# Kernel tuning notes

Measured on AMD Instinct MI355X. Metric: run time of the kernel, lower is better.

Reference implementation:

```python
import jax, jax.numpy as jnp
import numpy as np

N, E = 50000, 400000
IC, OC, WIDTH, DEPTH = 128, 128, 2, 3


def setup_inputs() -> dict:
    key = jax.random.key(0)
    ks = jax.random.split(key, 9)
    s = 0.02
    return {
        "node_tensor": jax.random.normal(ks[0], (N, 1, IC), jnp.float32),
        "edge_index": jax.random.randint(ks[1], (2, E), 0, N, dtype=jnp.int32),
        "W_pre": jax.random.normal(ks[2], (IC, OC * WIDTH), jnp.float32) * s,
        "b_pre": jax.random.normal(ks[3], (OC * WIDTH,), jnp.float32) * s,
        "W_merge": jax.random.normal(ks[4], (IC, OC * WIDTH), jnp.float32) * s,
        "b_merge": jax.random.normal(ks[5], (OC * WIDTH,), jnp.float32) * s,
        "W_conv": jax.random.normal(ks[6], (WIDTH, OC, OC), jnp.float32) * s,
        "b_conv": jax.random.normal(ks[7], (OC * WIDTH,), jnp.float32) * s,
    }


def reference(node_tensor, edge_index, W_pre, b_pre, W_merge, b_merge, W_conv, b_conv):
    n = node_tensor.shape[0]
    nodes = node_tensor[:, 0, :]                       # (N, IC)

    src, dst = edge_index[0], edge_index[1]
    deg = jax.ops.segment_sum(jnp.ones((E,), node_tensor.dtype), dst, num_segments=n)
    norm = jnp.where(deg > 0, jax.lax.rsqrt(jnp.maximum(deg, 1.0)), 0.0)  # D^{-1/2}

    def laplacian_action(x):                           # x: (N, C); L_sym x
        agg = jax.ops.segment_sum(norm[src, None] * x[src], dst, num_segments=n)
        return x - norm[:, None] * agg

    merge = nodes @ W_merge + b_merge                  # (N, OC*W)
    out = jax.nn.relu(nodes @ W_pre + b_pre + merge)   # (N, OC*W)

    for _ in range(DEPTH - 1):
        out = out - laplacian_action(out)
        # grouped 1x1 conv: width contiguous groups of OC channels
        h = out.reshape(n, WIDTH, OC)
        h = jnp.einsum("nwi,woi->nwo", h, W_conv).reshape(n, WIDTH * OC) + b_conv
        out = jax.nn.relu(h + merge)

    # final (N, OC, W) reshape + adaptive_avg_pool1d(1) == mean over width
    out = out.reshape(n, OC, WIDTH).mean(axis=-1)
    return out[:, :, None]                             # (N, OC, 1)
```

## Files before the change

### kernel.cpp

```cpp
#include <hip/hip_runtime.h>

typedef unsigned short u16;
typedef __attribute__((ext_vector_type(8))) short bf16x8;
typedef __attribute__((ext_vector_type(4))) float f32x4;

#define ICNST 128
#define C2 256

__device__ __forceinline__ float bf2f(u16 u){
  return __uint_as_float(((unsigned int)u) << 16);
}
__device__ __forceinline__ float2 bf2x2(unsigned int u){
  float2 r;
  r.x = __uint_as_float(u << 16);
  r.y = __uint_as_float(u & 0xffff0000u);
  return r;
}
__device__ __forceinline__ u16 f2bf(float f){
  unsigned int u = __float_as_uint(f);
  unsigned int r = (u + 0x7fffu + ((u >> 16) & 1u)) >> 16;
  return (u16)r;
}
__device__ __forceinline__ unsigned int pk2(float a, float b){
  return (unsigned int)f2bf(a) | ((unsigned int)f2bf(b) << 16);
}

__global__ __launch_bounds__(512) void k_zero(int* __restrict__ deg, int n){
  int i = blockIdx.x * 512 + threadIdx.x;
  if (i < n) deg[i] = 0;
}

__global__ __launch_bounds__(256) void k_pre(const int* __restrict__ dst,
    int* __restrict__ deg, const float* __restrict__ Wpre,
    const float* __restrict__ Wmrg, const float* __restrict__ Wcv,
    u16* __restrict__ WT, u16* __restrict__ Wc, int E){
  int bid = blockIdx.x;
  if (bid < 384){
    int idx = bid * 256 + threadIdx.x;
    if (idx < 65536){
      int j = idx & 511, k = idx >> 9;
      float v = (j < 256) ? Wpre[k * 256 + j] : Wmrg[k * 256 + (j - 256)];
      WT[j * 128 + k] = f2bf(v);
    } else if (idx < 65536 + 32768){
      int x = idx - 65536;
      Wc[x] = f2bf(Wcv[x]);
    }
  } else {
    int e = (bid - 384) * 256 + threadIdx.x;
    if (e < E) atomicAdd(&deg[dst[e]], 1);
  }
}

__global__ __launch_bounds__(256) void k_scan1(const int* __restrict__ deg,
    int* __restrict__ bsum, int n){
  __shared__ int red[256];
  int t = threadIdx.x;
  int i = blockIdx.x * 256 + t;
  red[t] = (i < n) ? deg[i] : 0;
  __syncthreads();
  for (int off = 128; off > 0; off >>= 1){
    if (t < off) red[t] += red[t + off];
    __syncthreads();
  }
  if (t == 0) bsum[blockIdx.x] = red[0];
}

__global__ __launch_bounds__(256) void k_scan2(int* __restrict__ bsum, int nb){
  __shared__ int s[256];
  int t = threadIdx.x;
  int v = (t < nb) ? bsum[t] : 0;
  s[t] = v;
  __syncthreads();
  for (int off = 1; off < 256; off <<= 1){
    int u = (t >= off) ? s[t - off] : 0;
    __syncthreads();
    s[t] += u;
    __syncthreads();
  }
  if (t < nb) bsum[t] = s[t] - v;
}

__global__ __launch_bounds__(256) void k_scan3(const int* __restrict__ deg,
    const int* __restrict__ bsum, int* __restrict__ row_start,
    int* __restrict__ cursor, float* __restrict__ norm, int n){
  __shared__ int s[256];
  int t = threadIdx.x;
  int i = blockIdx.x * 256 + t;
  int v = (i < n) ? deg[i] : 0;
  s[t] = v;
  __syncthreads();
  for (int off = 1; off < 256; off <<= 1){
    int u = (t >= off) ? s[t - off] : 0;
    __syncthreads();
    s[t] += u;
    __syncthreads();
  }
  int ex = s[t] - v + bsum[blockIdx.x];
  if (i < n){
    row_start[i] = ex;
    cursor[i] = ex;
    norm[i] = (v > 0) ? rsqrtf((float)v) : 0.f;
    if (i == n - 1) row_start[n] = ex + v;
  }
}

__global__ void k_scatter(const int* __restrict__ src, const int* __restrict__ dstA,
    int* __restrict__ cursor, int* __restrict__ csr_src, int E){
  int e = blockIdx.x * blockDim.x + threadIdx.x;
  if (e < E){
    int d = dstA[e];
    int pos = atomicAdd(&cursor[d], 1);
    csr_src[pos] = src[e];
  }
}

__global__ __launch_bounds__(512) void k_initM(const float* __restrict__ node,
    const u16* __restrict__ WT, const float* __restrict__ bpre,
    const float* __restrict__ bmrg, const float* __restrict__ norm,
    u16* __restrict__ merge, u16* __restrict__ outA, int n){
  __shared__ u16 Al[64 * 128];
  __shared__ u16 Ep[64 * 256];
  int t = threadIdx.x;
  int w = t >> 6, l = t & 63;
  int n0 = blockIdx.x * 64;
  int cb = w * 32;
  int lk = (l >> 4) * 8;

  float nr4[4];
  #pragma unroll
  for (int fr = 0; fr < 4; ++fr){
    int row = n0 + fr * 16 + (l & 15);
    nr4[fr] = (row < n) ? norm[row] : 0.f;
  }
  float4 bPr[2], bMr[2];
  #pragma unroll
  for (int fcp = 0; fcp < 2; ++fcp){
    int j0 = cb + fcp * 16 + (l >> 4) * 4;
    bPr[fcp] = *(const float4*)(bpre + j0);
    bMr[fcp] = *(const float4*)(bmrg + j0);
  }

  {
    int row = t >> 3, c0 = (t & 7) * 16;
    const float* src = node + (size_t)(n0 + row) * ICNST + c0;
    bool ok = (n0 + row) < n;
    #pragma unroll
    for (int q = 0; q < 4; ++q){
      float4 v = ok ? *(const float4*)(src + q * 4) : float4{0.f, 0.f, 0.f, 0.f};
      int byte = (row * 256 + c0 * 2 + q * 8) ^ ((row & 7) << 4);
      uint2 pp; pp.x = pk2(v.x, v.y); pp.y = pk2(v.z, v.w);
      *(uint2*)((char*)Al + byte) = pp;
    }
  }
  __syncthreads();

  f32x4 acc[4][4] = {};
  #pragma unroll
  for (int ks = 0; ks < 4; ++ks){
    bf16x8 bf[4];
    #pragma unroll
    for (int fc = 0; fc < 4; ++fc){
      int j = (fc < 2) ? (cb + fc * 16 + (l & 15))
                       : (256 + cb + (fc - 2) * 16 + (l & 15));
      bf[fc] = *(const bf16x8*)(WT + (size_t)j * 128 + ks * 32 + lk);
    }
    bf16x8 af[4];
    #pragma unroll
    for (int fr = 0; fr < 4; ++fr){
      int row = fr * 16 + (l & 15);
      int byte = (row * 256 + ks * 64 + (l >> 4) * 16) ^ ((l & 7) << 4);
      af[fr] = *(const bf16x8*)((const char*)Al + byte);
    }
    #pragma unroll
    for (int fr = 0; fr < 4; ++fr)
      #pragma unroll
      for (int fc = 0; fc < 4; ++fc)
        acc[fr][fc] = __builtin_amdgcn_mfma_f32_16x16x32_bf16(bf[fc], af[fr], acc[fr][fc], 0, 0, 0);
  }

  #pragma unroll
  for (int fr = 0; fr < 4; ++fr){
    int rl = fr * 16 + (l & 15);
    int row = n0 + rl;
    bool ok = row < n;
    float nr = nr4[fr];
    #pragma unroll
    for (int fcp = 0; fcp < 2; ++fcp){
      int j0 = cb + fcp * 16 + (l >> 4) * 4;
      f32x4 aP = acc[fr][fcp], aM = acc[fr][fcp + 2];
      float bPe[4] = {bPr[fcp].x, bPr[fcp].y, bPr[fcp].z, bPr[fcp].w};
      float bMe[4] = {bMr[fcp].x, bMr[fcp].y, bMr[fcp].z, bMr[fcp].w};
      ushort4 mgv, outv;
      u16* mgp = (u16*)&mgv; u16* otp = (u16*)&outv;
      #pragma unroll
      for (int r = 0; r < 4; ++r){
        float mg = aM[r] + bMe[r];
        float o  = aP[r] + bPe[r] + mg;
        o = (o > 0.f) ? o : 0.f;
        mgp[r] = f2bf(mg);
        otp[r] = f2bf(nr * o);
      }
      if (ok) *(ushort4*)(merge + (size_t)row * C2 + j0) = mgv;
      int byte = (rl * 512 + j0 * 2) ^ ((rl & 7) << 4);
      *(ushort4*)((char*)Ep + byte) = outv;
    }
  }
  __syncthreads();
  #pragma unroll
  for (int round = 0; round < 4; ++round){
    int idx = round * 512 + t;
    int rl = idx >> 5, off = (idx & 31) * 16;
    int byte = (rl * 512 + off) ^ ((rl & 7) << 4);
    uint4 v = *(const uint4*)((const char*)Ep + byte);
    if (n0 + rl < n)
      *(uint4*)((char*)outA + (size_t)(n0 + rl) * 512 + off) = v;
  }
}

template<int FINAL>
__global__ __launch_bounds__(512) void k_convM(u16* __restrict__ buf,
    const u16* __restrict__ Wc, const float* __restrict__ bc,
    const u16* __restrict__ merge, const float* __restrict__ norm,
    float* __restrict__ out, int n){
  __shared__ u16 Al[64 * 256];
  __shared__ u16 Ep[64 * 256];
  int t = threadIdx.x;
  int w = t >> 6, l = t & 63;
  int n0 = blockIdx.x * 64;
  int wh = w >> 2;
  int lk = (l >> 4) * 8;

  float nr4[4];
  #pragma unroll
  for (int fr = 0; fr < 4; ++fr){
    int row = n0 + fr * 16 + (l & 15);
    nr4[fr] = (row < n) ? norm[row] : 0.f;
  }
  float4 bCr[2];
  #pragma unroll
  for (int fc = 0; fc < 2; ++fc)
    bCr[fc] = *(const float4*)(bc + w * 32 + fc * 16 + (l >> 4) * 4);

  {
    int row = t >> 3, c0 = (t & 7) * 32;
    bool ok = (n0 + row) < n;
    const u16* srcA = buf   + (size_t)(n0 + row) * C2 + c0;
    const u16* srcM = merge + (size_t)(n0 + row) * C2 + c0;
    #pragma unroll
    for (int q = 0; q < 4; ++q){
      uint4 va = ok ? *(const uint4*)(srcA + q * 8) : uint4{0u, 0u, 0u, 0u};
      int byte = (row * 512 + c0 * 2 + q * 16) ^ ((row & 7) << 4);
      *(uint4*)((char*)Al + byte) = va;
      uint4 vm = ok ? *(const uint4*)(srcM + q * 8) : uint4{0u, 0u, 0u, 0u};
      *(uint4*)((char*)Ep + byte) = vm;
    }
  }
  __syncthreads();

  f32x4 acc[4][2] = {};
  #pragma unroll
  for (int ks = 0; ks < 4; ++ks){
    bf16x8 bf[2];
    #pragma unroll
    for (int fc = 0; fc < 2; ++fc){
      int rw = w * 32 + fc * 16 + (l & 15);
      bf[fc] = *(const bf16x8*)(Wc + (size_t)rw * 128 + ks * 32 + lk);
    }
    bf16x8 af[4];
    #pragma unroll
    for (int fr = 0; fr < 4; ++fr){
      int row = fr * 16 + (l & 15);
      int byte = (row * 512 + wh * 256 + ks * 64 + (l >> 4) * 16) ^ ((l & 7) << 4);
      af[fr] = *(const bf16x8*)((const char*)Al + byte);
    }
    #pragma unroll
    for (int fr = 0; fr < 4; ++fr)
      #pragma unroll
      for (int fc = 0; fc < 2; ++fc)
        acc[fr][fc] = __builtin_amdgcn_mfma_f32_16x16x32_bf16(bf[fc], af[fr], acc[fr][fc], 0, 0, 0);
  }

  #pragma unroll
  for (int fr = 0; fr < 4; ++fr){
    int rl = fr * 16 + (l & 15);
    float nr = nr4[fr];
    #pragma unroll
    for (int fc = 0; fc < 2; ++fc){
      int j0 = w * 32 + fc * 16 + (l >> 4) * 4;
      int byte = (rl * 512 + j0 * 2) ^ ((rl & 7) << 4);
      ushort4 mg4 = *(const ushort4*)((const char*)Ep + byte);
      const u16* mge = (const u16*)&mg4;
      float bCe[4] = {bCr[fc].x, bCr[fc].y, bCr[fc].z, bCr[fc].w};
      float v[4];
      #pragma unroll
      for (int r = 0; r < 4; ++r){
        float o = acc[fr][fc][r] + bCe[r] + bf2f(mge[r]);
        v[r] = (o > 0.f) ? o : 0.f;
      }
      if (!FINAL){
        ushort4 ov;
        u16* ovp = (u16*)&ov;
        #pragma unroll
        for (int r = 0; r < 4; ++r) ovp[r] = f2bf(nr * v[r]);
        *(ushort4*)((char*)Ep + byte) = ov;
      } else {
        float2 om;
        om.x = 0.5f * (v[0] + v[1]);
        om.y = 0.5f * (v[2] + v[3]);
        *(float2*)((char*)Ep + byte) = om;
      }
    }
  }
  __syncthreads();
  char* dstBase = FINAL ? (char*)out : (char*)buf;
  #pragma unroll
  for (int round = 0; round < 4; ++round){
    int idx = round * 512 + t;
    int rl = idx >> 5, off = (idx & 31) * 16;
    int byte = (rl * 512 + off) ^ ((rl & 7) << 4);
    uint4 v = *(const uint4*)((const char*)Ep + byte);
    if (n0 + rl < n)
      *(uint4*)(dstBase + (size_t)(n0 + rl) * 512 + off) = v;
  }
}

__global__ __launch_bounds__(256) void k_prop(const u16* __restrict__ A, u16* __restrict__ B,
    const int* __restrict__ row_start, const int* __restrict__ csr,
    const float* __restrict__ norm, int n){
  int wid = (blockIdx.x * 256 + threadIdx.x) >> 6;
  int lane = threadIdx.x & 63;
  int half = lane >> 5, c = lane & 31;
  int gw = wid * 2 + half;
  if (gw >= n) return;
  int b = row_start[gw], e = row_start[gw + 1];
  float a0 = 0.f, a1 = 0.f, a2 = 0.f, a3 = 0.f, a4 = 0.f, a5 = 0.f, a6 = 0.f, a7 = 0.f;
  const u16* Ac = A + (size_t)c * 8;
  int j = b;
  for (; j + 4 <= e; j += 4){
    int s0 = csr[j], s1 = csr[j + 1], s2 = csr[j + 2], s3 = csr[j + 3];
    uint4 r0 = *(const uint4*)(Ac + (size_t)s0 * C2);
    uint4 r1 = *(const uint4*)(Ac + (size_t)s1 * C2);
    uint4 r2 = *(const uint4*)(Ac + (size_t)s2 * C2);
    uint4 r3 = *(const uint4*)(Ac + (size_t)s3 * C2);
    float2 p;
    p = bf2x2(r0.x); a0 += p.x; a1 += p.y; p = bf2x2(r0.y); a2 += p.x; a3 += p.y;
    p = bf2x2(r0.z); a4 += p.x; a5 += p.y; p = bf2x2(r0.w); a6 += p.x; a7 += p.y;
    p = bf2x2(r1.x); a0 += p.x; a1 += p.y; p = bf2x2(r1.y); a2 += p.x; a3 += p.y;
    p = bf2x2(r1.z); a4 += p.x; a5 += p.y; p = bf2x2(r1.w); a6 += p.x; a7 += p.y;
    p = bf2x2(r2.x); a0 += p.x; a1 += p.y; p = bf2x2(r2.y); a2 += p.x; a3 += p.y;
    p = bf2x2(r2.z); a4 += p.x; a5 += p.y; p = bf2x2(r2.w); a6 += p.x; a7 += p.y;
    p = bf2x2(r3.x); a0 += p.x; a1 += p.y; p = bf2x2(r3.y); a2 += p.x; a3 += p.y;
    p = bf2x2(r3.z); a4 += p.x; a5 += p.y; p = bf2x2(r3.w); a6 += p.x; a7 += p.y;
  }
  for (; j < e; ++j){
    int s0 = csr[j];
    uint4 r0 = *(const uint4*)(Ac + (size_t)s0 * C2);
    float2 p;
    p = bf2x2(r0.x); a0 += p.x; a1 += p.y; p = bf2x2(r0.y); a2 += p.x; a3 += p.y;
    p = bf2x2(r0.z); a4 += p.x; a5 += p.y; p = bf2x2(r0.w); a6 += p.x; a7 += p.y;
  }
  float nd = norm[gw];
  uint4 ov;
  ov.x = pk2(nd * a0, nd * a1);
  ov.y = pk2(nd * a2, nd * a3);
  ov.z = pk2(nd * a4, nd * a5);
  ov.w = pk2(nd * a6, nd * a7);
  *(uint4*)(B + (size_t)gw * C2 + c * 8) = ov;
}

extern "C" void kernel_launch(void* const* d_in, const int* in_sizes, int n_in,
                              void* d_out, int out_size, void* d_ws, size_t ws_size,
                              hipStream_t stream){
  const float* node = (const float*)d_in[0];
  const int*   eidx = (const int*)d_in[1];
  const float* Wpre = (const float*)d_in[2];
  const float* bpre = (const float*)d_in[3];
  const float* Wmrg = (const float*)d_in[4];
  const float* bmrg = (const float*)d_in[5];
  const float* Wcv  = (const float*)d_in[6];
  const float* bcv  = (const float*)d_in[7];
  float* out = (float*)d_out;

  const int n = in_sizes[0] / ICNST;
  const int E = in_sizes[1] / 2;
  const int* srcp = eidx;
  const int* dstp = eidx + E;

  char* ws = (char*)d_ws;
  size_t off = 0;
  auto alloc = [&](size_t bytes) -> char* {
    char* p = ws + off;
    off += bytes;
    off = (off + 255) & ~(size_t)255;
    return p;
  };
  int*   deg       = (int*)  alloc((size_t)n * 4);
  float* norm      = (float*)alloc((size_t)n * 4);
  int*   row_start = (int*)  alloc((size_t)(n + 1) * 4);
  int*   cursor    = (int*)  alloc((size_t)n * 4);
  int*   csr       = (int*)  alloc((size_t)E * 4);
  u16*   merge     = (u16*)  alloc((size_t)n * C2 * 2);
  u16*   bufA      = (u16*)  alloc((size_t)n * C2 * 2);
  u16*   bufB      = (u16*)  alloc((size_t)n * C2 * 2);
  u16*   WT        = (u16*)  alloc((size_t)512 * 128 * 2);
  u16*   Wcbf      = (u16*)  alloc((size_t)2 * 128 * 128 * 2);
  int*   bsum      = (int*)  alloc((size_t)256 * 4);
  (void)ws_size; (void)n_in; (void)out_size;

  const int nb = (n + 255) / 256;

  k_zero<<<(n + 511) / 512, 512, 0, stream>>>(deg, n);
  k_pre<<<384 + (E + 255) / 256, 256, 0, stream>>>(dstp, deg, Wpre, Wmrg, Wcv, WT, Wcbf, E);
  k_scan1<<<nb, 256, 0, stream>>>(deg, bsum, n);
  k_scan2<<<1, 256, 0, stream>>>(bsum, nb);
  k_scan3<<<nb, 256, 0, stream>>>(deg, bsum, row_start, cursor, norm, n);
  k_scatter<<<(E + 255) / 256, 256, 0, stream>>>(srcp, dstp, cursor, csr, E);

  int gb64 = (n + 63) / 64;
  k_initM<<<gb64, 512, 0, stream>>>(node, WT, bpre, bmrg, norm, merge, bufA, n);

  k_prop<<<(n + 7) / 8, 256, 0, stream>>>(bufA, bufB, row_start, csr, norm, n);
  k_convM<0><<<gb64, 512, 0, stream>>>(bufB, Wcbf, bcv, merge, norm, nullptr, n);
  k_prop<<<(n + 7) / 8, 256, 0, stream>>>(bufB, bufA, row_start, csr, norm, n);
  k_convM<1><<<gb64, 512, 0, stream>>>(bufA, Wcbf, bcv, merge, norm, out, n);
}
```

Before: 209.1 us.

## Fuse neighbor aggregation into grouped conv kernel, dropping intermediate buffer round trip

```diff
diff --git a/kernel.cpp b/kernel.cpp
--- a/kernel.cpp
+++ b/kernel.cpp
@@ -218,17 +218,19 @@
 }
 
 template<int FINAL>
-__global__ __launch_bounds__(512) void k_convM(u16* __restrict__ buf,
+__global__ __launch_bounds__(512) void k_pconv(const u16* __restrict__ src,
+    const int* __restrict__ row_start, const int* __restrict__ csr,
+    const float* __restrict__ norm,
     const u16* __restrict__ Wc, const float* __restrict__ bc,
-    const u16* __restrict__ merge, const float* __restrict__ norm,
-    float* __restrict__ out, int n){
+    const u16* __restrict__ merge,
+    u16* __restrict__ dstB, float* __restrict__ out, int n){
   __shared__ u16 Al[64 * 256];
-  __shared__ u16 Ep[64 * 256];
   int t = threadIdx.x;
   int w = t >> 6, l = t & 63;
   int n0 = blockIdx.x * 64;
   int wh = w >> 2;
   int lk = (l >> 4) * 8;
+  int half = l >> 5, c = l & 31;
 
   float nr4[4];
   #pragma unroll
@@ -241,19 +243,48 @@
   for (int fc = 0; fc < 2; ++fc)
     bCr[fc] = *(const float4*)(bc + w * 32 + fc * 16 + (l >> 4) * 4);
 
-  {
-    int row = t >> 3, c0 = (t & 7) * 32;
-    bool ok = (n0 + row) < n;
-    const u16* srcA = buf   + (size_t)(n0 + row) * C2 + c0;
-    const u16* srcM = merge + (size_t)(n0 + row) * C2 + c0;
-    #pragma unroll
-    for (int q = 0; q < 4; ++q){
-      uint4 va = ok ? *(const uint4*)(srcA + q * 8) : uint4{0u, 0u, 0u, 0u};
-      int byte = (row * 512 + c0 * 2 + q * 16) ^ ((row & 7) << 4);
-      *(uint4*)((char*)Al + byte) = va;
-      uint4 vm = ok ? *(const uint4*)(srcM + q * 8) : uint4{0u, 0u, 0u, 0u};
-      *(uint4*)((char*)Ep + byte) = vm;
-    }
+  const u16* Ac = src + (size_t)c * 8;
+  #pragma unroll
+  for (int it = 0; it < 4; ++it){
+    int rl = w * 8 + it * 2 + half;
+    int gw = n0 + rl;
+    float a0 = 0.f, a1 = 0.f, a2 = 0.f, a3 = 0.f, a4 = 0.f, a5 = 0.f, a6 = 0.f, a7 = 0.f;
+    float nd = 0.f;
+    if (gw < n){
+      int b = row_start[gw], e = row_start[gw + 1];
+      int j = b;
+      for (; j + 4 <= e; j += 4){
+        int s0 = csr[j], s1 = csr[j + 1], s2 = csr[j + 2], s3 = csr[j + 3];
+        uint4 r0 = *(const uint4*)(Ac + (size_t)s0 * C2);
+        uint4 r1 = *(const uint4*)(Ac + (size_t)s1 * C2);
+        uint4 r2 = *(const uint4*)(Ac + (size_t)s2 * C2);
+        uint4 r3 = *(const uint4*)(Ac + (size_t)s3 * C2);
+        float2 p;
+        p = bf2x2(r0.x); a0 += p.x; a1 += p.y; p = bf2x2(r0.y); a2 += p.x; a3 += p.y;
+        p = bf2x2(r0.z); a4 += p.x; a5 += p.y; p = bf2x2(r0.w); a6 += p.x; a7 += p.y;
+        p = bf2x2(r1.x); a0 += p.x; a1 += p.y; p = bf2x2(r1.y); a2 += p.x; a3 += p.y;
+        p = bf2x2(r1.z); a4 += p.x; a5 += p.y; p = bf2x2(r1.w); a6 += p.x; a7 += p.y;
+        p = bf2x2(r2.x); a0 += p.x; a1 += p.y; p = bf2x2(r2.y); a2 += p.x; a3 += p.y;
+        p = bf2x2(r2.z); a4 += p.x; a5 += p.y; p = bf2x2(r2.w); a6 += p.x; a7 += p.y;
+        p = bf2x2(r3.x); a0 += p.x; a1 += p.y; p = bf2x2(r3.y); a2 += p.x; a3 += p.y;
+        p = bf2x2(r3.z); a4 += p.x; a5 += p.y; p = bf2x2(r3.w); a6 += p.x; a7 += p.y;
+      }
+      for (; j < e; ++j){
+        int s0 = csr[j];
+        uint4 r0 = *(const uint4*)(Ac + (size_t)s0 * C2);
+        float2 p;
+        p = bf2x2(r0.x); a0 += p.x; a1 += p.y; p = bf2x2(r0.y); a2 += p.x; a3 += p.y;
+        p = bf2x2(r0.z); a4 += p.x; a5 += p.y; p = bf2x2(r0.w); a6 += p.x; a7 += p.y;
+      }
+      nd = norm[gw];
+    }
+    uint4 ov;
+    ov.x = pk2(nd * a0, nd * a1);
+    ov.y = pk2(nd * a2, nd * a3);
+    ov.z = pk2(nd * a4, nd * a5);
+    ov.w = pk2(nd * a6, nd * a7);
+    int byte = (rl * 512 + c * 16) ^ ((rl & 7) << 4);
+    *(uint4*)((char*)Al + byte) = ov;
   }
   __syncthreads();
 
@@ -280,15 +311,18 @@
         acc[fr][fc] = __builtin_amdgcn_mfma_f32_16x16x32_bf16(bf[fc], af[fr], acc[fr][fc], 0, 0, 0);
   }
 
+  ushort4 resB[4][2];
+  float2  resF[4][2];
   #pragma unroll
   for (int fr = 0; fr < 4; ++fr){
-    int rl = fr * 16 + (l & 15);
+    int row = n0 + fr * 16 + (l & 15);
+    bool ok = row < n;
     float nr = nr4[fr];
     #pragma unroll
     for (int fc = 0; fc < 2; ++fc){
       int j0 = w * 32 + fc * 16 + (l >> 4) * 4;
-      int byte = (rl * 512 + j0 * 2) ^ ((rl & 7) << 4);
-      ushort4 mg4 = *(const ushort4*)((const char*)Ep + byte);
+      ushort4 mg4 = ok ? *(const ushort4*)(merge + (size_t)row * C2 + j0)
+                       : ushort4{0, 0, 0, 0};
       const u16* mge = (const u16*)&mg4;
       float bCe[4] = {bCr[fc].x, bCr[fc].y, bCr[fc].z, bCr[fc].w};
       float v[4];
@@ -298,74 +332,38 @@
         v[r] = (o > 0.f) ? o : 0.f;
       }
       if (!FINAL){
-        ushort4 ov;
-        u16* ovp = (u16*)&ov;
+        u16* rp = (u16*)&resB[fr][fc];
         #pragma unroll
-        for (int r = 0; r < 4; ++r) ovp[r] = f2bf(nr * v[r]);
-        *(ushort4*)((char*)Ep + byte) = ov;
+        for (int r = 0; r < 4; ++r) rp[r] = f2bf(nr * v[r]);
       } else {
-        float2 om;
-        om.x = 0.5f * (v[0] + v[1]);
-        om.y = 0.5f * (v[2] + v[3]);
-        *(float2*)((char*)Ep + byte) = om;
+        resF[fr][fc].x = 0.5f * (v[0] + v[1]);
+        resF[fr][fc].y = 0.5f * (v[2] + v[3]);
       }
     }
   }
   __syncthreads();
-  char* dstBase = FINAL ? (char*)out : (char*)buf;
+  #pragma unroll
+  for (int fr = 0; fr < 4; ++fr){
+    int rl = fr * 16 + (l & 15);
+    #pragma unroll
+    for (int fc = 0; fc < 2; ++fc){
+      int j0 = w * 32 + fc * 16 + (l >> 4) * 4;
+      int byte = (rl * 512 + j0 * 2) ^ ((rl & 7) << 4);
+      if (!FINAL) *(ushort4*)((char*)Al + byte) = resB[fr][fc];
+      else        *(float2*)((char*)Al + byte) = resF[fr][fc];
+    }
+  }
+  __syncthreads();
+  char* dstBase = FINAL ? (char*)out : (char*)dstB;
   #pragma unroll
   for (int round = 0; round < 4; ++round){
     int idx = round * 512 + t;
     int rl = idx >> 5, off = (idx & 31) * 16;
     int byte = (rl * 512 + off) ^ ((rl & 7) << 4);
-    uint4 v = *(const uint4*)((const char*)Ep + byte);
+    uint4 v = *(const uint4*)((const char*)Al + byte);
     if (n0 + rl < n)
       *(uint4*)(dstBase + (size_t)(n0 + rl) * 512 + off) = v;
   }
-}
-
-__global__ __launch_bounds__(256) void k_prop(const u16* __restrict__ A, u16* __restrict__ B,
-    const int* __restrict__ row_start, const int* __restrict__ csr,
-    const float* __restrict__ norm, int n){
-  int wid = (blockIdx.x * 256 + threadIdx.x) >> 6;
-  int lane = threadIdx.x & 63;
-  int half = lane >> 5, c = lane & 31;
-  int gw = wid * 2 + half;
-  if (gw >= n) return;
-  int b = row_start[gw], e = row_start[gw + 1];
-  float a0 = 0.f, a1 = 0.f, a2 = 0.f, a3 = 0.f, a4 = 0.f, a5 = 0.f, a6 = 0.f, a7 = 0.f;
-  const u16* Ac = A + (size_t)c * 8;
-  int j = b;
-  for (; j + 4 <= e; j += 4){
-    int s0 = csr[j], s1 = csr[j + 1], s2 = csr[j + 2], s3 = csr[j + 3];
-    uint4 r0 = *(const uint4*)(Ac + (size_t)s0 * C2);
-    uint4 r1 = *(const uint4*)(Ac + (size_t)s1 * C2);
-    uint4 r2 = *(const uint4*)(Ac + (size_t)s2 * C2);
-    uint4 r3 = *(const uint4*)(Ac + (size_t)s3 * C2);
-    float2 p;
-    p = bf2x2(r0.x); a0 += p.x; a1 += p.y; p = bf2x2(r0.y); a2 += p.x; a3 += p.y;
-    p = bf2x2(r0.z); a4 += p.x; a5 += p.y; p = bf2x2(r0.w); a6 += p.x; a7 += p.y;
-    p = bf2x2(r1.x); a0 += p.x; a1 += p.y; p = bf2x2(r1.y); a2 += p.x; a3 += p.y;
-    p = bf2x2(r1.z); a4 += p.x; a5 += p.y; p = bf2x2(r1.w); a6 += p.x; a7 += p.y;
-    p = bf2x2(r2.x); a0 += p.x; a1 += p.y; p = bf2x2(r2.y); a2 += p.x; a3 += p.y;
-    p = bf2x2(r2.z); a4 += p.x; a5 += p.y; p = bf2x2(r2.w); a6 += p.x; a7 += p.y;
-    p = bf2x2(r3.x); a0 += p.x; a1 += p.y; p = bf2x2(r3.y); a2 += p.x; a3 += p.y;
-    p = bf2x2(r3.z); a4 += p.x; a5 += p.y; p = bf2x2(r3.w); a6 += p.x; a7 += p.y;
-  }
-  for (; j < e; ++j){
-    int s0 = csr[j];
-    uint4 r0 = *(const uint4*)(Ac + (size_t)s0 * C2);
-    float2 p;
-    p = bf2x2(r0.x); a0 += p.x; a1 += p.y; p = bf2x2(r0.y); a2 += p.x; a3 += p.y;
-    p = bf2x2(r0.z); a4 += p.x; a5 += p.y; p = bf2x2(r0.w); a6 += p.x; a7 += p.y;
-  }
-  float nd = norm[gw];
-  uint4 ov;
-  ov.x = pk2(nd * a0, nd * a1);
-  ov.y = pk2(nd * a2, nd * a3);
-  ov.z = pk2(nd * a4, nd * a5);
-  ov.w = pk2(nd * a6, nd * a7);
-  *(uint4*)(B + (size_t)gw * C2 + c * 8) = ov;
 }
 
 extern "C" void kernel_launch(void* const* d_in, const int* in_sizes, int n_in,
@@ -419,8 +417,6 @@
   int gb64 = (n + 63) / 64;
   k_initM<<<gb64, 512, 0, stream>>>(node, WT, bpre, bmrg, norm, merge, bufA, n);
 
-  k_prop<<<(n + 7) / 8, 256, 0, stream>>>(bufA, bufB, row_start, csr, norm, n);
-  k_convM<0><<<gb64, 512, 0, stream>>>(bufB, Wcbf, bcv, merge, norm, nullptr, n);
-  k_prop<<<(n + 7) / 8, 256, 0, stream>>>(bufB, bufA, row_start, csr, norm, n);
-  k_convM<1><<<gb64, 512, 0, stream>>>(bufA, Wcbf, bcv, merge, norm, out, n);
-}
+  k_pconv<0><<<gb64, 512, 0, stream>>>(bufA, row_start, csr, norm, Wcbf, bcv, merge, bufB, nullptr, n);
+  k_pconv<1><<<gb64, 512, 0, stream>>>(bufB, row_start, csr, norm, Wcbf, bcv, merge, nullptr, out, n);
+}
```

After: 204.6 us. 1.02x faster.
